# Kernel tuning notes

Hardware: AMD Instinct MI355X
Metric: run time of the kernel (lower is better)

## Reference

```python
import jax, jax.numpy as jnp
import numpy as np
import math

NUM_BUCKETS = 32
MAX_DISTANCE = 128
NUM_HEADS = 16
D_MODEL = 1024
HEAD_DIM = D_MODEL // NUM_HEADS


def _relative_position_bucket(relative_position, num_buckets=NUM_BUCKETS, max_distance=MAX_DISTANCE):
    # bidirectional=False path of the original
    rp = -jnp.minimum(relative_position, 0)  # non-negative distances
    max_exact = num_buckets // 2
    is_small = rp < max_exact
    rp_safe = jnp.maximum(rp, 1).astype(jnp.float32)
    rp_if_large = max_exact + (
        jnp.log(rp_safe / max_exact) / math.log(max_distance / max_exact) * (num_buckets - max_exact)
    ).astype(jnp.int32)
    rp_if_large = jnp.minimum(rp_if_large, num_buckets - 1)
    return jnp.where(is_small, rp, rp_if_large)


def relative_bias(rab_weight, q_len, k_len):
    ctx = jnp.arange(q_len)[:, None]
    mem = jnp.arange(k_len)[None, :]
    buckets = _relative_position_bucket(mem - ctx)  # [Q, K]
    vals = rab_weight[buckets]                       # [Q, K, H]
    return jnp.transpose(vals, (2, 0, 1))[None]      # [1, H, Q, K]


def setup_inputs() -> dict:
    key = jax.random.key(0)
    k1, k2, k3, k4 = jax.random.split(key, 4)
    B, S = 4, 2048
    return {
        "v": jax.random.normal(k1, (B, S, D_MODEL), dtype=jnp.float32),
        "k": jax.random.normal(k2, (B, S, D_MODEL), dtype=jnp.float32),
        "q": jax.random.normal(k3, (B, S, D_MODEL), dtype=jnp.float32),
        "rab_weight": jax.random.normal(k4, (NUM_BUCKETS, NUM_HEADS), dtype=jnp.float32),
    }


def reference(v, k, q, rab_weight):
    B, S, _ = q.shape
    def split(x):
        return jnp.transpose(x.reshape(B, S, NUM_HEADS, HEAD_DIM), (0, 2, 1, 3))  # [B,H,S,D]
    qh, kh, vh = split(q), split(k), split(v)
    scores = jnp.einsum("bhqd,bhkd->bhqk", qh, kh)          # [B,H,S,S]
    scores = scores + relative_bias(rab_weight, S, S)        # add relative bias
    av = jnp.einsum("bhqk,bhkd->bhqd", jax.nn.silu(scores), vh)
    return jnp.transpose(av, (0, 2, 1, 3)).reshape(B, S, D_MODEL)
```

## Files before the change

kernel.cpp:

```cpp
#include <hip/hip_runtime.h>

#define SEQ 2048
#define NH 16
#define HD 64
#define DMODEL 1024

typedef short bf16x8 __attribute__((ext_vector_type(8)));
typedef float f32x16 __attribute__((ext_vector_type(16)));

union FragU {
    bf16x8 v;
    uint2 u2[2];
    unsigned int w[4];
    unsigned short s[8];
};

#if __has_builtin(__builtin_amdgcn_cvt_pk_bf16_f32)
typedef __bf16 v2bf_t __attribute__((ext_vector_type(2)));
__device__ __forceinline__ unsigned int pack_bf16(float lo, float hi) {
    union { v2bf_t h; unsigned int u; } cv;
    cv.h = __builtin_amdgcn_cvt_pk_bf16_f32(lo, hi);
    return cv.u;
}
#else
__device__ __forceinline__ unsigned int pack_bf16(float lo, float hi) {
    unsigned int a = __float_as_uint(lo) + 0x8000u;
    unsigned int b = __float_as_uint(hi) + 0x8000u;
    return __builtin_amdgcn_perm(b, a, 0x07060302);
}
#endif

#define EXP_SCALE 1.44269504f
#define LN2       0.69314718f

__global__ __launch_bounds__(512, 4)
void paa_kernel(const float* __restrict__ Vg, const float* __restrict__ Kg,
                const float* __restrict__ Qg, const float* __restrict__ RW,
                float* __restrict__ Og)
{
    __shared__ __align__(16) unsigned short KsLds[2][64 * 68];
    __shared__ __align__(16) unsigned short VtLds[2][64 * 68];
    __shared__ float btab[128];

    const int tid  = threadIdx.x;
    const int lane = tid & 63;
    const int wave = tid >> 6;
    const int half = lane >> 5;
    const int l31  = lane & 31;

    const int bid  = blockIdx.x;
    const int bh   = bid & 63;
    const int qt   = bid >> 6;
    const int b    = bh >> 4;
    const int head = bh & 15;

    const int q0w = qt * 256 + wave * 32;

    if (tid < 128) {
        int rp = tid;
        int bucket;
        if (rp < 16) bucket = rp;
        else {
            int big = 16 + (int)(logf((float)rp * 0.0625f) * 7.6943736f);
            bucket = big < 31 ? big : 31;
        }
        btab[tid] = RW[bucket * NH + head] * EXP_SCALE;
    }

    FragU qf[4];
    {
        const float* qrow = Qg + (size_t)(b * SEQ + q0w + l31) * DMODEL + head * HD;
        #pragma unroll
        for (int kf = 0; kf < 4; ++kf) {
            int dd = kf * 16 + half * 8;
            float4 x0 = *(const float4*)(qrow + dd);
            float4 x1 = *(const float4*)(qrow + dd + 4);
            FragU f;
            f.w[0] = pack_bf16(x0.x * EXP_SCALE, x0.y * EXP_SCALE);
            f.w[1] = pack_bf16(x0.z * EXP_SCALE, x0.w * EXP_SCALE);
            f.w[2] = pack_bf16(x1.x * EXP_SCALE, x1.y * EXP_SCALE);
            f.w[3] = pack_bf16(x1.z * EXP_SCALE, x1.w * EXP_SCALE);
            qf[kf] = f;
        }
    }

    f32x16 oacc[2];
    #pragma unroll
    for (int n = 0; n < 2; ++n)
        #pragma unroll
        for (int r = 0; r < 16; ++r) oacc[n][r] = 0.0f;

    const int krow = tid >> 4;
    const int c4   = tid & 15;
    const int kc2  = tid >> 4;
    const int d4   = tid & 15;

    const float* kp = Kg + (size_t)(b * SEQ + krow) * DMODEL + head * HD + c4 * 4;
    const float* vp = Vg + (size_t)(b * SEQ + kc2 * 2) * DMODEL + head * HD + d4 * 4;

    {
        float4 k0 = *(const float4*)(kp);
        float4 k1 = *(const float4*)(kp + (size_t)32 * DMODEL);
        float4 v0 = *(const float4*)(vp);
        float4 v1 = *(const float4*)(vp + DMODEL);
        kp += (size_t)64 * DMODEL;
        vp += (size_t)64 * DMODEL;
        uint2 w;
        w.x = pack_bf16(k0.x, k0.y); w.y = pack_bf16(k0.z, k0.w);
        *(uint2*)&KsLds[0][krow * 68 + c4 * 4] = w;
        w.x = pack_bf16(k1.x, k1.y); w.y = pack_bf16(k1.z, k1.w);
        *(uint2*)&KsLds[0][(krow + 32) * 68 + c4 * 4] = w;
        *(unsigned int*)&VtLds[0][(d4 * 4 + 0) * 68 + kc2 * 2] = pack_bf16(v0.x, v1.x);
        *(unsigned int*)&VtLds[0][(d4 * 4 + 1) * 68 + kc2 * 2] = pack_bf16(v0.y, v1.y);
        *(unsigned int*)&VtLds[0][(d4 * 4 + 2) * 68 + kc2 * 2] = pack_bf16(v0.z, v1.z);
        *(unsigned int*)&VtLds[0][(d4 * 4 + 3) * 68 + kc2 * 2] = pack_bf16(v0.w, v1.w);
    }
    __syncthreads();

    const float bias_d0  = btab[0];
    const float bias_far = btab[127];

    #pragma unroll 2
    for (int it = 0; it < 32; ++it) {
        const int cur = it & 1;
        const int kcb = it * 64;
        const unsigned short* Ks = KsLds[cur];
        const unsigned short* Vt = VtLds[cur];
        const bool pre = (it < 31);

        float4 k0, k1, v0, v1;
        if (pre) {
            k0 = *(const float4*)(kp);
            k1 = *(const float4*)(kp + (size_t)32 * DMODEL);
            v0 = *(const float4*)(vp);
            v1 = *(const float4*)(vp + DMODEL);
            kp += (size_t)64 * DMODEL;
            vp += (size_t)64 * DMODEL;
        }

        f32x16 st[2];
        #pragma unroll
        for (int t = 0; t < 2; ++t) {
            const int kcmin = kcb + t * 32;
            if (q0w + 31 - kcmin <= 0) {
                #pragma unroll
                for (int r = 0; r < 16; ++r) st[t][r] = bias_d0;
            } else if (q0w - (kcmin + 31) >= 113) {
                #pragma unroll
                for (int r = 0; r < 16; ++r) st[t][r] = bias_far;
            } else {
                const int dql = q0w + l31 - kcmin - 4 * half;
                #pragma unroll
                for (int r = 0; r < 16; ++r) {
                    int dv = dql - ((r & 3) + 8 * (r >> 2));
                    dv = dv < 0 ? 0 : (dv > 127 ? 127 : dv);
                    st[t][r] = btab[dv];
                }
            }
        }

        __builtin_amdgcn_s_setprio(1);
        #pragma unroll
        for (int kf = 0; kf < 4; ++kf) {
            FragU ka0, ka1;
            {
                int off = l31 * 68 + kf * 16 + half * 8;
                ka0.u2[0] = *(const uint2*)&Ks[off];
                ka0.u2[1] = *(const uint2*)&Ks[off + 4];
                off += 32 * 68;
                ka1.u2[0] = *(const uint2*)&Ks[off];
                ka1.u2[1] = *(const uint2*)&Ks[off + 4];
            }
            st[0] = __builtin_amdgcn_mfma_f32_32x32x16_bf16(ka0.v, qf[kf].v, st[0], 0, 0, 0);
            st[1] = __builtin_amdgcn_mfma_f32_32x32x16_bf16(ka1.v, qf[kf].v, st[1], 0, 0, 0);
        }
        __builtin_amdgcn_s_setprio(0);

        FragU pf[4];
        #pragma unroll
        for (int t = 0; t < 2; ++t) {
            float vals[16];
            #pragma unroll
            for (int r = 0; r < 16; ++r) {
                float x = st[t][r];
                float e = __builtin_amdgcn_exp2f(-x);
                vals[r] = x * __builtin_amdgcn_rcpf(1.0f + e);
            }
            #pragma unroll
            for (int j = 0; j < 4; ++j)
                pf[t * 2].w[j]     = pack_bf16(vals[2 * j], vals[2 * j + 1]);
            #pragma unroll
            for (int j = 0; j < 4; ++j)
                pf[t * 2 + 1].w[j] = pack_bf16(vals[8 + 2 * j], vals[9 + 2 * j]);
        }

        if (pre) {
            const int nb = cur ^ 1;
            uint2 w;
            w.x = pack_bf16(k0.x, k0.y); w.y = pack_bf16(k0.z, k0.w);
            *(uint2*)&KsLds[nb][krow * 68 + c4 * 4] = w;
            w.x = pack_bf16(k1.x, k1.y); w.y = pack_bf16(k1.z, k1.w);
            *(uint2*)&KsLds[nb][(krow + 32) * 68 + c4 * 4] = w;
            *(unsigned int*)&VtLds[nb][(d4 * 4 + 0) * 68 + kc2 * 2] = pack_bf16(v0.x, v1.x);
            *(unsigned int*)&VtLds[nb][(d4 * 4 + 1) * 68 + kc2 * 2] = pack_bf16(v0.y, v1.y);
            *(unsigned int*)&VtLds[nb][(d4 * 4 + 2) * 68 + kc2 * 2] = pack_bf16(v0.z, v1.z);
            *(unsigned int*)&VtLds[nb][(d4 * 4 + 3) * 68 + kc2 * 2] = pack_bf16(v0.w, v1.w);
        }

        #pragma unroll
        for (int f = 0; f < 4; ++f) {
            #pragma unroll
            for (int n = 0; n < 2; ++n) {
                FragU vf;
                int off = (n * 32 + l31) * 68 + f * 16 + half * 4;
                vf.u2[0] = *(const uint2*)&Vt[off];
                vf.u2[1] = *(const uint2*)&Vt[off + 8];
                oacc[n] = __builtin_amdgcn_mfma_f32_32x32x16_bf16(pf[f].v, vf.v, oacc[n], 0, 0, 0);
            }
        }

        if (pre) __syncthreads();
    }

    float* obase = Og + (size_t)(b * SEQ) * DMODEL + head * HD;
    #pragma unroll
    for (int r = 0; r < 16; ++r) {
        int q = q0w + (r & 3) + 8 * (r >> 2) + 4 * half;
        float* orow = obase + (size_t)q * DMODEL;
        #pragma unroll
        for (int n = 0; n < 2; ++n)
            orow[n * 32 + l31] = oacc[n][r] * LN2;
    }
}

extern "C" void kernel_launch(void* const* d_in, const int* in_sizes, int n_in,
                              void* d_out, int out_size, void* d_ws, size_t ws_size,
                              hipStream_t stream) {
    const float* v  = (const float*)d_in[0];
    const float* k  = (const float*)d_in[1];
    const float* q  = (const float*)d_in[2];
    const float* rw = (const float*)d_in[3];
    float* out = (float*)d_out;
    paa_kernel<<<dim3(512), dim3(512), 0, stream>>>(v, k, q, rw, out);
}
```

Baseline: 214.7 us.

## Split score tile into two halves interleaved with PV MFMAs; batch SiLU reciprocals

Restructures each key-tile iteration so the two 32-column score subtiles are computed and activated one at a time, with the PV MFMAs for the first half issued before the second half's QK. This should cut live registers, since only one score accumulator is held at a time, and give the scheduler a chance to overlap SiLU ALU work with MFMA execution. SiLU now shares a single reciprocal across four values through products, and clamps the exponent to avoid overflow. The shared reciprocal adds multiplies and may cost some precision.

```diff
diff --git a/kernel.cpp b/kernel.cpp
--- a/kernel.cpp
+++ b/kernel.cpp
@@ -32,6 +32,51 @@
 
 #define EXP_SCALE 1.44269504f
 #define LN2       0.69314718f
+
+__device__ __forceinline__ void silu_pack16(const f32x16& st, FragU& plo, FragU& phi) {
+    float vals[16];
+    #pragma unroll
+    for (int g = 0; g < 4; ++g) {
+        float x0 = st[4 * g + 0], x1 = st[4 * g + 1];
+        float x2 = st[4 * g + 2], x3 = st[4 * g + 3];
+        float e0 = __builtin_amdgcn_exp2f(fminf(30.0f, -x0));
+        float e1 = __builtin_amdgcn_exp2f(fminf(30.0f, -x1));
+        float e2 = __builtin_amdgcn_exp2f(fminf(30.0f, -x2));
+        float e3 = __builtin_amdgcn_exp2f(fminf(30.0f, -x3));
+        float a0 = 1.0f + e0, a1 = 1.0f + e1;
+        float a2 = 1.0f + e2, a3 = 1.0f + e3;
+        float p01 = a0 * a1, p23 = a2 * a3;
+        float R   = __builtin_amdgcn_rcpf(p01 * p23);
+        float R01 = R * p23, R23 = R * p01;
+        vals[4 * g + 0] = x0 * a1 * R01;
+        vals[4 * g + 1] = x1 * a0 * R01;
+        vals[4 * g + 2] = x2 * a3 * R23;
+        vals[4 * g + 3] = x3 * a2 * R23;
+    }
+    #pragma unroll
+    for (int j = 0; j < 4; ++j) plo.w[j] = pack_bf16(vals[2 * j], vals[2 * j + 1]);
+    #pragma unroll
+    for (int j = 0; j < 4; ++j) phi.w[j] = pack_bf16(vals[8 + 2 * j], vals[9 + 2 * j]);
+}
+
+__device__ __forceinline__ void bias_init(f32x16& st, int q0w, int l31, int half, int kcmin,
+                                          float bias_d0, float bias_far, const float* btab) {
+    if (q0w + 31 - kcmin <= 0) {
+        #pragma unroll
+        for (int r = 0; r < 16; ++r) st[r] = bias_d0;
+    } else if (q0w - (kcmin + 31) >= 113) {
+        #pragma unroll
+        for (int r = 0; r < 16; ++r) st[r] = bias_far;
+    } else {
+        const int dql = q0w + l31 - kcmin - 4 * half;
+        #pragma unroll
+        for (int r = 0; r < 16; ++r) {
+            int dv = dql - ((r & 3) + 8 * (r >> 2));
+            dv = dv < 0 ? 0 : (dv > 127 ? 127 : dv);
+            st[r] = btab[dv];
+        }
+    }
+}
 
 __global__ __launch_bounds__(512, 4)
 void paa_kernel(const float* __restrict__ Vg, const float* __restrict__ Kg,
@@ -138,60 +183,61 @@
             vp += (size_t)64 * DMODEL;
         }
 
-        f32x16 st[2];
-        #pragma unroll
-        for (int t = 0; t < 2; ++t) {
-            const int kcmin = kcb + t * 32;
-            if (q0w + 31 - kcmin <= 0) {
-                #pragma unroll
-                for (int r = 0; r < 16; ++r) st[t][r] = bias_d0;
-            } else if (q0w - (kcmin + 31) >= 113) {
-                #pragma unroll
-                for (int r = 0; r < 16; ++r) st[t][r] = bias_far;
-            } else {
-                const int dql = q0w + l31 - kcmin - 4 * half;
-                #pragma unroll
-                for (int r = 0; r < 16; ++r) {
-                    int dv = dql - ((r & 3) + 8 * (r >> 2));
-                    dv = dv < 0 ? 0 : (dv > 127 ? 127 : dv);
-                    st[t][r] = btab[dv];
-                }
+        FragU pf0, pf1, pf2, pf3;
+
+        {
+            f32x16 st;
+            bias_init(st, q0w, l31, half, kcb, bias_d0, bias_far, btab);
+            FragU ka[4];
+            #pragma unroll
+            for (int kf = 0; kf < 4; ++kf) {
+                int off = l31 * 68 + kf * 16 + half * 8;
+                ka[kf].u2[0] = *(const uint2*)&Ks[off];
+                ka[kf].u2[1] = *(const uint2*)&Ks[off + 4];
             }
+            __builtin_amdgcn_s_setprio(1);
+            #pragma unroll
+            for (int kf = 0; kf < 4; ++kf)
+                st = __builtin_amdgcn_mfma_f32_32x32x16_bf16(ka[kf].v, qf[kf].v, st, 0, 0, 0);
+            __builtin_amdgcn_s_setprio(0);
+            silu_pack16(st, pf0, pf1);
         }
 
         __builtin_amdgcn_s_setprio(1);
         #pragma unroll
-        for (int kf = 0; kf < 4; ++kf) {
-            FragU ka0, ka1;
-            {
-                int off = l31 * 68 + kf * 16 + half * 8;
-                ka0.u2[0] = *(const uint2*)&Ks[off];
-                ka0.u2[1] = *(const uint2*)&Ks[off + 4];
-                off += 32 * 68;
-                ka1.u2[0] = *(const uint2*)&Ks[off];
-                ka1.u2[1] = *(const uint2*)&Ks[off + 4];
+        for (int n = 0; n < 2; ++n) {
+            FragU vf;
+            int off = (n * 32 + l31) * 68 + half * 4;
+            vf.u2[0] = *(const uint2*)&Vt[off];
+            vf.u2[1] = *(const uint2*)&Vt[off + 8];
+            oacc[n] = __builtin_amdgcn_mfma_f32_32x32x16_bf16(pf0.v, vf.v, oacc[n], 0, 0, 0);
+        }
+        #pragma unroll
+        for (int n = 0; n < 2; ++n) {
+            FragU vf;
+            int off = (n * 32 + l31) * 68 + 16 + half * 4;
+            vf.u2[0] = *(const uint2*)&Vt[off];
+            vf.u2[1] = *(const uint2*)&Vt[off + 8];
+            oacc[n] = __builtin_amdgcn_mfma_f32_32x32x16_bf16(pf1.v, vf.v, oacc[n], 0, 0, 0);
+        }
+        __builtin_amdgcn_s_setprio(0);
+
+        {
+            f32x16 st;
+            bias_init(st, q0w, l31, half, kcb + 32, bias_d0, bias_far, btab);
+            FragU ka[4];
+            #pragma unroll
+            for (int kf = 0; kf < 4; ++kf) {
+                int off = (32 + l31) * 68 + kf * 16 + half * 8;
+                ka[kf].u2[0] = *(const uint2*)&Ks[off];
+                ka[kf].u2[1] = *(const uint2*)&Ks[off + 4];
             }
-            st[0] = __builtin_amdgcn_mfma_f32_32x32x16_bf16(ka0.v, qf[kf].v, st[0], 0, 0, 0);
-            st[1] = __builtin_amdgcn_mfma_f32_32x32x16_bf16(ka1.v, qf[kf].v, st[1], 0, 0, 0);
-        }
-        __builtin_amdgcn_s_setprio(0);
-
-        FragU pf[4];
-        #pragma unroll
-        for (int t = 0; t < 2; ++t) {
-            float vals[16];
-            #pragma unroll
-            for (int r = 0; r < 16; ++r) {
-                float x = st[t][r];
-                float e = __builtin_amdgcn_exp2f(-x);
-                vals[r] = x * __builtin_amdgcn_rcpf(1.0f + e);
-            }
-            #pragma unroll
-            for (int j = 0; j < 4; ++j)
-                pf[t * 2].w[j]     = pack_bf16(vals[2 * j], vals[2 * j + 1]);
-            #pragma unroll
-            for (int j = 0; j < 4; ++j)
-                pf[t * 2 + 1].w[j] = pack_bf16(vals[8 + 2 * j], vals[9 + 2 * j]);
+            __builtin_amdgcn_s_setprio(1);
+            #pragma unroll
+            for (int kf = 0; kf < 4; ++kf)
+                st = __builtin_amdgcn_mfma_f32_32x32x16_bf16(ka[kf].v, qf[kf].v, st, 0, 0, 0);
+            __builtin_amdgcn_s_setprio(0);
+            silu_pack16(st, pf2, pf3);
         }
 
         if (pre) {
@@ -207,17 +253,24 @@
             *(unsigned int*)&VtLds[nb][(d4 * 4 + 3) * 68 + kc2 * 2] = pack_bf16(v0.w, v1.w);
         }
 
-        #pragma unroll
-        for (int f = 0; f < 4; ++f) {
-            #pragma unroll
-            for (int n = 0; n < 2; ++n) {
-                FragU vf;
-                int off = (n * 32 + l31) * 68 + f * 16 + half * 4;
-                vf.u2[0] = *(const uint2*)&Vt[off];
-                vf.u2[1] = *(const uint2*)&Vt[off + 8];
-                oacc[n] = __builtin_amdgcn_mfma_f32_32x32x16_bf16(pf[f].v, vf.v, oacc[n], 0, 0, 0);
-            }
-        }
+        __builtin_amdgcn_s_setprio(1);
+        #pragma unroll
+        for (int n = 0; n < 2; ++n) {
+            FragU vf;
+            int off = (n * 32 + l31) * 68 + 32 + half * 4;
+            vf.u2[0] = *(const uint2*)&Vt[off];
+            vf.u2[1] = *(const uint2*)&Vt[off + 8];
+            oacc[n] = __builtin_amdgcn_mfma_f32_32x32x16_bf16(pf2.v, vf.v, oacc[n], 0, 0, 0);
+        }
+        #pragma unroll
+        for (int n = 0; n < 2; ++n) {
+            FragU vf;
+            int off = (n * 32 + l31) * 68 + 48 + half * 4;
+            vf.u2[0] = *(const uint2*)&Vt[off];
+            vf.u2[1] = *(const uint2*)&Vt[off + 8];
+            oacc[n] = __builtin_amdgcn_mfma_f32_32x32x16_bf16(pf3.v, vf.v, oacc[n], 0, 0, 0);
+        }
+        __builtin_amdgcn_s_setprio(0);
 
         if (pre) __syncthreads();
     }
```

Result: slower. 237.3 us (+10.5%).

## Double K/V tile to 128 keys and interleave QK, SiLU and PV per sub-tile

Applied to the files above, without the earlier changes.

Each iteration now stages 128 keys instead of 64, which halves the number of barriers and loop iterations. Within an iteration the work is split into 32-key sub-tiles, so each QK MFMA pair is followed directly by its SiLU and PV MFMAs, and the K and V global loads are issued at different points to spread memory traffic. LDS use roughly doubles (about 70KB per block), which may limit how many blocks fit per CU and raise register pressure.

```diff
diff --git a/kernel.cpp b/kernel.cpp
--- a/kernel.cpp
+++ b/kernel.cpp
@@ -33,13 +33,16 @@
 #define EXP_SCALE 1.44269504f
 #define LN2       0.69314718f
 
+#define KST 68
+#define VST 138
+
 __global__ __launch_bounds__(512, 4)
 void paa_kernel(const float* __restrict__ Vg, const float* __restrict__ Kg,
                 const float* __restrict__ Qg, const float* __restrict__ RW,
                 float* __restrict__ Og)
 {
-    __shared__ __align__(16) unsigned short KsLds[2][64 * 68];
-    __shared__ __align__(16) unsigned short VtLds[2][64 * 68];
+    __shared__ __align__(16) unsigned short KsLds[2][128 * KST];
+    __shared__ __align__(16) unsigned short VtLds[2][64 * VST];
     __shared__ float btab[128];
 
     const int tid  = threadIdx.x;
@@ -99,125 +102,168 @@
     const float* vp = Vg + (size_t)(b * SEQ + kc2 * 2) * DMODEL + head * HD + d4 * 4;
 
     {
-        float4 k0 = *(const float4*)(kp);
-        float4 k1 = *(const float4*)(kp + (size_t)32 * DMODEL);
-        float4 v0 = *(const float4*)(vp);
-        float4 v1 = *(const float4*)(vp + DMODEL);
-        kp += (size_t)64 * DMODEL;
-        vp += (size_t)64 * DMODEL;
+        float4 kx0 = *(const float4*)(kp);
+        float4 kx1 = *(const float4*)(kp + (size_t)32 * DMODEL);
+        float4 kx2 = *(const float4*)(kp + (size_t)64 * DMODEL);
+        float4 kx3 = *(const float4*)(kp + (size_t)96 * DMODEL);
+        float4 va0 = *(const float4*)(vp);
+        float4 vb0 = *(const float4*)(vp + DMODEL);
+        float4 va1 = *(const float4*)(vp + (size_t)64 * DMODEL);
+        float4 vb1 = *(const float4*)(vp + (size_t)64 * DMODEL + DMODEL);
+        kp += (size_t)128 * DMODEL;
+        vp += (size_t)128 * DMODEL;
         uint2 w;
-        w.x = pack_bf16(k0.x, k0.y); w.y = pack_bf16(k0.z, k0.w);
-        *(uint2*)&KsLds[0][krow * 68 + c4 * 4] = w;
-        w.x = pack_bf16(k1.x, k1.y); w.y = pack_bf16(k1.z, k1.w);
-        *(uint2*)&KsLds[0][(krow + 32) * 68 + c4 * 4] = w;
-        *(unsigned int*)&VtLds[0][(d4 * 4 + 0) * 68 + kc2 * 2] = pack_bf16(v0.x, v1.x);
-        *(unsigned int*)&VtLds[0][(d4 * 4 + 1) * 68 + kc2 * 2] = pack_bf16(v0.y, v1.y);
-        *(unsigned int*)&VtLds[0][(d4 * 4 + 2) * 68 + kc2 * 2] = pack_bf16(v0.z, v1.z);
-        *(unsigned int*)&VtLds[0][(d4 * 4 + 3) * 68 + kc2 * 2] = pack_bf16(v0.w, v1.w);
+        w.x = pack_bf16(kx0.x, kx0.y); w.y = pack_bf16(kx0.z, kx0.w);
+        *(uint2*)&KsLds[0][(krow +  0) * KST + c4 * 4] = w;
+        w.x = pack_bf16(kx1.x, kx1.y); w.y = pack_bf16(kx1.z, kx1.w);
+        *(uint2*)&KsLds[0][(krow + 32) * KST + c4 * 4] = w;
+        w.x = pack_bf16(kx2.x, kx2.y); w.y = pack_bf16(kx2.z, kx2.w);
+        *(uint2*)&KsLds[0][(krow + 64) * KST + c4 * 4] = w;
+        w.x = pack_bf16(kx3.x, kx3.y); w.y = pack_bf16(kx3.z, kx3.w);
+        *(uint2*)&KsLds[0][(krow + 96) * KST + c4 * 4] = w;
+        *(unsigned int*)&VtLds[0][(d4 * 4 + 0) * VST + kc2 * 2]      = pack_bf16(va0.x, vb0.x);
+        *(unsigned int*)&VtLds[0][(d4 * 4 + 1) * VST + kc2 * 2]      = pack_bf16(va0.y, vb0.y);
+        *(unsigned int*)&VtLds[0][(d4 * 4 + 2) * VST + kc2 * 2]      = pack_bf16(va0.z, vb0.z);
+        *(unsigned int*)&VtLds[0][(d4 * 4 + 3) * VST + kc2 * 2]      = pack_bf16(va0.w, vb0.w);
+        *(unsigned int*)&VtLds[0][(d4 * 4 + 0) * VST + 64 + kc2 * 2] = pack_bf16(va1.x, vb1.x);
+        *(unsigned int*)&VtLds[0][(d4 * 4 + 1) * VST + 64 + kc2 * 2] = pack_bf16(va1.y, vb1.y);
+        *(unsigned int*)&VtLds[0][(d4 * 4 + 2) * VST + 64 + kc2 * 2] = pack_bf16(va1.z, vb1.z);
+        *(unsigned int*)&VtLds[0][(d4 * 4 + 3) * VST + 64 + kc2 * 2] = pack_bf16(va1.w, vb1.w);
     }
     __syncthreads();
 
     const float bias_d0  = btab[0];
     const float bias_far = btab[127];
 
-    #pragma unroll 2
-    for (int it = 0; it < 32; ++it) {
-        const int cur = it & 1;
-        const int kcb = it * 64;
-        const unsigned short* Ks = KsLds[cur];
-        const unsigned short* Vt = VtLds[cur];
-        const bool pre = (it < 31);
-
-        float4 k0, k1, v0, v1;
-        if (pre) {
-            k0 = *(const float4*)(kp);
-            k1 = *(const float4*)(kp + (size_t)32 * DMODEL);
-            v0 = *(const float4*)(vp);
-            v1 = *(const float4*)(vp + DMODEL);
-            kp += (size_t)64 * DMODEL;
-            vp += (size_t)64 * DMODEL;
-        }
-
-        f32x16 st[2];
+    auto qk2 = [&](const unsigned short* Ks, int ubase, int kcb_u,
+                   f32x16& s0, f32x16& s1) {
         #pragma unroll
         for (int t = 0; t < 2; ++t) {
-            const int kcmin = kcb + t * 32;
+            f32x16& st = t ? s1 : s0;
+            const int kcmin = kcb_u + t * 32;
             if (q0w + 31 - kcmin <= 0) {
                 #pragma unroll
-                for (int r = 0; r < 16; ++r) st[t][r] = bias_d0;
+                for (int r = 0; r < 16; ++r) st[r] = bias_d0;
             } else if (q0w - (kcmin + 31) >= 113) {
                 #pragma unroll
-                for (int r = 0; r < 16; ++r) st[t][r] = bias_far;
+                for (int r = 0; r < 16; ++r) st[r] = bias_far;
             } else {
                 const int dql = q0w + l31 - kcmin - 4 * half;
                 #pragma unroll
                 for (int r = 0; r < 16; ++r) {
                     int dv = dql - ((r & 3) + 8 * (r >> 2));
                     dv = dv < 0 ? 0 : (dv > 127 ? 127 : dv);
-                    st[t][r] = btab[dv];
+                    st[r] = btab[dv];
                 }
             }
         }
-
         __builtin_amdgcn_s_setprio(1);
         #pragma unroll
         for (int kf = 0; kf < 4; ++kf) {
             FragU ka0, ka1;
-            {
-                int off = l31 * 68 + kf * 16 + half * 8;
-                ka0.u2[0] = *(const uint2*)&Ks[off];
-                ka0.u2[1] = *(const uint2*)&Ks[off + 4];
-                off += 32 * 68;
-                ka1.u2[0] = *(const uint2*)&Ks[off];
-                ka1.u2[1] = *(const uint2*)&Ks[off + 4];
-            }
-            st[0] = __builtin_amdgcn_mfma_f32_32x32x16_bf16(ka0.v, qf[kf].v, st[0], 0, 0, 0);
-            st[1] = __builtin_amdgcn_mfma_f32_32x32x16_bf16(ka1.v, qf[kf].v, st[1], 0, 0, 0);
+            int off = (ubase + l31) * KST + kf * 16 + half * 8;
+            ka0.u2[0] = *(const uint2*)&Ks[off];
+            ka0.u2[1] = *(const uint2*)&Ks[off + 4];
+            off += 32 * KST;
+            ka1.u2[0] = *(const uint2*)&Ks[off];
+            ka1.u2[1] = *(const uint2*)&Ks[off + 4];
+            s0 = __builtin_amdgcn_mfma_f32_32x32x16_bf16(ka0.v, qf[kf].v, s0, 0, 0, 0);
+            s1 = __builtin_amdgcn_mfma_f32_32x32x16_bf16(ka1.v, qf[kf].v, s1, 0, 0, 0);
         }
         __builtin_amdgcn_s_setprio(0);
-
-        FragU pf[4];
-        #pragma unroll
-        for (int t = 0; t < 2; ++t) {
-            float vals[16];
-            #pragma unroll
-            for (int r = 0; r < 16; ++r) {
-                float x = st[t][r];
-                float e = __builtin_amdgcn_exp2f(-x);
-                vals[r] = x * __builtin_amdgcn_rcpf(1.0f + e);
-            }
-            #pragma unroll
-            for (int j = 0; j < 4; ++j)
-                pf[t * 2].w[j]     = pack_bf16(vals[2 * j], vals[2 * j + 1]);
-            #pragma unroll
-            for (int j = 0; j < 4; ++j)
-                pf[t * 2 + 1].w[j] = pack_bf16(vals[8 + 2 * j], vals[9 + 2 * j]);
-        }
+    };
+
+    auto siluPack = [&](const f32x16& st, FragU& lo, FragU& hi) {
+        float vals[16];
+        #pragma unroll
+        for (int r = 0; r < 16; ++r) {
+            float x = st[r];
+            float e = __builtin_amdgcn_exp2f(-x);
+            vals[r] = x * __builtin_amdgcn_rcpf(1.0f + e);
+        }
+        #pragma unroll
+        for (int j = 0; j < 4; ++j) lo.w[j] = pack_bf16(vals[2 * j], vals[2 * j + 1]);
+        #pragma unroll
+        for (int j = 0; j < 4; ++j) hi.w[j] = pack_bf16(vals[8 + 2 * j], vals[9 + 2 * j]);
+    };
+
+    auto pv1 = [&](const unsigned short* Vt, int ubase, int fbase, const FragU& pf) {
+        #pragma unroll
+        for (int n = 0; n < 2; ++n) {
+            FragU vf;
+            int off = (n * 32 + l31) * VST + ubase + fbase * 16 + half * 4;
+            vf.u2[0] = *(const uint2*)&Vt[off];
+            vf.u2[1] = *(const uint2*)&Vt[off + 8];
+            oacc[n] = __builtin_amdgcn_mfma_f32_32x32x16_bf16(pf.v, vf.v, oacc[n], 0, 0, 0);
+        }
+    };
+
+    #pragma unroll 2
+    for (int it = 0; it < 16; ++it) {
+        const int cur = it & 1;
+        const int kcb = it * 128;
+        const unsigned short* Ks = KsLds[cur];
+        const unsigned short* Vt = VtLds[cur];
+        const bool pre = (it < 15);
+
+        float4 kx0, kx1, kx2, kx3;
+        if (pre) {
+            kx0 = *(const float4*)(kp);
+            kx1 = *(const float4*)(kp + (size_t)32 * DMODEL);
+            kx2 = *(const float4*)(kp + (size_t)64 * DMODEL);
+            kx3 = *(const float4*)(kp + (size_t)96 * DMODEL);
+            kp += (size_t)128 * DMODEL;
+        }
+
+        FragU pf0, pf1, pf2, pf3;
+        f32x16 s0, s1;
+
+        qk2(Ks, 0, kcb, s0, s1);
+        siluPack(s0, pf0, pf1);
+        pv1(Vt, 0, 0, pf0);
+        pv1(Vt, 0, 1, pf1);
+        siluPack(s1, pf2, pf3);
+        pv1(Vt, 0, 2, pf2);
+        pv1(Vt, 0, 3, pf3);
+
+        float4 va0, vb0, va1, vb1;
+        if (pre) {
+            va0 = *(const float4*)(vp);
+            vb0 = *(const float4*)(vp + DMODEL);
+            va1 = *(const float4*)(vp + (size_t)64 * DMODEL);
+            vb1 = *(const float4*)(vp + (size_t)64 * DMODEL + DMODEL);
+            vp += (size_t)128 * DMODEL;
+        }
+
+        qk2(Ks, 64, kcb + 64, s0, s1);
+        siluPack(s0, pf0, pf1);
+        pv1(Vt, 64, 0, pf0);
+        pv1(Vt, 64, 1, pf1);
 
         if (pre) {
             const int nb = cur ^ 1;
             uint2 w;
-            w.x = pack_bf16(k0.x, k0.y); w.y = pack_bf16(k0.z, k0.w);
-            *(uint2*)&KsLds[nb][krow * 68 + c4 * 4] = w;
-            w.x = pack_bf16(k1.x, k1.y); w.y = pack_bf16(k1.z, k1.w);
-            *(uint2*)&KsLds[nb][(krow + 32) * 68 + c4 * 4] = w;
-            *(unsigned int*)&VtLds[nb][(d4 * 4 + 0) * 68 + kc2 * 2] = pack_bf16(v0.x, v1.x);
-            *(unsigned int*)&VtLds[nb][(d4 * 4 + 1) * 68 + kc2 * 2] = pack_bf16(v0.y, v1.y);
-            *(unsigned int*)&VtLds[nb][(d4 * 4 + 2) * 68 + kc2 * 2] = pack_bf16(v0.z, v1.z);
-            *(unsigned int*)&VtLds[nb][(d4 * 4 + 3) * 68 + kc2 * 2] = pack_bf16(v0.w, v1.w);
-        }
-
-        #pragma unroll
-        for (int f = 0; f < 4; ++f) {
-            #pragma unroll
-            for (int n = 0; n < 2; ++n) {
-                FragU vf;
-                int off = (n * 32 + l31) * 68 + f * 16 + half * 4;
-                vf.u2[0] = *(const uint2*)&Vt[off];
-                vf.u2[1] = *(const uint2*)&Vt[off + 8];
-                oacc[n] = __builtin_amdgcn_mfma_f32_32x32x16_bf16(pf[f].v, vf.v, oacc[n], 0, 0, 0);
-            }
-        }
+            w.x = pack_bf16(kx0.x, kx0.y); w.y = pack_bf16(kx0.z, kx0.w);
+            *(uint2*)&KsLds[nb][(krow +  0) * KST + c4 * 4] = w;
+            w.x = pack_bf16(kx1.x, kx1.y); w.y = pack_bf16(kx1.z, kx1.w);
+            *(uint2*)&KsLds[nb][(krow + 32) * KST + c4 * 4] = w;
+            w.x = pack_bf16(kx2.x, kx2.y); w.y = pack_bf16(kx2.z, kx2.w);
+            *(uint2*)&KsLds[nb][(krow + 64) * KST + c4 * 4] = w;
+            w.x = pack_bf16(kx3.x, kx3.y); w.y = pack_bf16(kx3.z, kx3.w);
+            *(uint2*)&KsLds[nb][(krow + 96) * KST + c4 * 4] = w;
+            *(unsigned int*)&VtLds[nb][(d4 * 4 + 0) * VST + kc2 * 2]      = pack_bf16(va0.x, vb0.x);
+            *(unsigned int*)&VtLds[nb][(d4 * 4 + 1) * VST + kc2 * 2]      = pack_bf16(va0.y, vb0.y);
+            *(unsigned int*)&VtLds[nb][(d4 * 4 + 2) * VST + kc2 * 2]      = pack_bf16(va0.z, vb0.z);
+            *(unsigned int*)&VtLds[nb][(d4 * 4 + 3) * VST + kc2 * 2]      = pack_bf16(va0.w, vb0.w);
+            *(unsigned int*)&VtLds[nb][(d4 * 4 + 0) * VST + 64 + kc2 * 2] = pack_bf16(va1.x, vb1.x);
+            *(unsigned int*)&VtLds[nb][(d4 * 4 + 1) * VST + 64 + kc2 * 2] = pack_bf16(va1.y, vb1.y);
+            *(unsigned int*)&VtLds[nb][(d4 * 4 + 2) * VST + 64 + kc2 * 2] = pack_bf16(va1.z, vb1.z);
+            *(unsigned int*)&VtLds[nb][(d4 * 4 + 3) * VST + 64 + kc2 * 2] = pack_bf16(va1.w, vb1.w);
+        }
+
+        siluPack(s1, pf2, pf3);
+        pv1(Vt, 64, 2, pf2);
+        pv1(Vt, 64, 3, pf3);
 
         if (pre) __syncthreads();
     }
```

Result: slower. 379.8 us (+76.9%).
